# Performance work log

Measured on AMD Instinct MI355X. Metric: run time of the kernel, lower is better.

## Reference

```python
import jax, jax.numpy as jnp
import numpy as np

B, T, D = 2, 1024, 2048
N, K, H = 16, 4, 128          # num_heads, num_kv_heads, head_dim
TC = 1024                     # cached tokens
S = TC + T
MAX_WAVELENGTH = 10000.0
BIG_NEG = -2.3819763e38


def _apply_rope(x, positions):
    """RoPE: positions [B,L] applied to x [B,L,heads,H]."""
    half = x.shape[-1] // 2
    freq_exponents = (2.0 / x.shape[-1]) * jnp.arange(half, dtype=jnp.float32)
    timescale = MAX_WAVELENGTH ** freq_exponents                      # [H/2]
    radians = (positions.astype(jnp.float32)[..., None] / timescale)[..., None, :]  # [B,L,1,H/2]
    sin, cos = jnp.sin(radians), jnp.cos(radians)
    x1, x2 = jnp.split(x, 2, axis=-1)
    res = jnp.concatenate([x1 * cos - x2 * sin, x2 * cos + x1 * sin], axis=-1)
    return res.astype(x.dtype)


def setup_inputs() -> dict:
    key = jax.random.key(0)
    ks = jax.random.split(key, 8)
    x = jax.random.normal(ks[0], (B, T, D), dtype=jnp.float32)
    # new tokens sit right after the cache
    positions = jnp.broadcast_to(TC + jnp.arange(T, dtype=jnp.int32), (B, T))
    # causal mask over [cache + new]: query t may attend to keys s <= TC + t
    s_idx = jnp.arange(S)[None, :]
    t_idx = jnp.arange(T)[:, None]
    attn_mask = jnp.broadcast_to((s_idx <= TC + t_idx)[None, None, :, :], (B, 1, T, S))
    cache_k = jax.random.normal(ks[1], (B, TC, K, H), dtype=jnp.float32)
    cache_v = jax.random.normal(ks[2], (B, TC, K, H), dtype=jnp.float32)
    # lecun-normal-ish fan-in scaling (fan_in = D for projections, N*H for output)
    w_q = jax.random.normal(ks[3], (N, D, H), dtype=jnp.float32) * (D ** -0.5)
    w_kv = jax.random.normal(ks[4], (2, K, D, H), dtype=jnp.float32) * (D ** -0.5)
    w_out = jax.random.normal(ks[5], (N, H, D), dtype=jnp.float32) * ((N * H) ** -0.5)
    return {"x": x, "positions": positions, "attn_mask": attn_mask,
            "cache_k": cache_k, "cache_v": cache_v,
            "w_q": w_q, "w_kv": w_kv, "w_out": w_out}


def reference(x, positions, attn_mask, cache_k, cache_v, w_q, w_kv, w_out):
    dtype = x.dtype
    # projections (GQA path: num_kv_heads != num_heads)
    q = jnp.einsum('BTD,NDH->BTNH', x, w_q.astype(dtype))
    kv = jnp.einsum('BSD,CKDH->CBSKH', x, w_kv.astype(dtype))
    k_new, v_new = kv[0], kv[1]
    # inline RoPE + query scaling
    q = _apply_rope(q, positions) * (H ** -0.5)
    k_new = _apply_rope(k_new, positions)
    # KV-cache concat
    k = jnp.concatenate([cache_k, k_new], axis=1)   # [B,S,K,H]
    v = jnp.concatenate([cache_v, v_new], axis=1)
    # group heads: B T (K G) H -> B T K G H
    G = N // K
    qg = q.reshape(q.shape[0], q.shape[1], K, G, H)
    logits = jnp.einsum('BTKGH,BSKH->BKGTS', qg, k,
                        preferred_element_type=jnp.float32)
    masked = jnp.where(attn_mask[:, :, None, :, :], logits, BIG_NEG)
    probs = jax.nn.softmax(masked, axis=-1).astype(dtype)
    enc = jnp.einsum('BKGTS,BSKH->BTKGH', probs, v)
    enc = enc.reshape(enc.shape[0], enc.shape[1], N, H)  # B T (K G) H
    out = jnp.einsum('BTNH,NHD->BTD', enc, w_out.astype(dtype))
    return out, k, v
```

## Files before the change

### kernel.cpp

```cpp
#include <hip/hip_runtime.h>

#define B_  2
#define T_  1024
#define D_  2048
#define NH  16
#define KH  4
#define HD  128
#define TC_ 1024
#define S_  2048

typedef __bf16 bf16x4v __attribute__((ext_vector_type(4)));
typedef __bf16 bf16x8v __attribute__((ext_vector_type(8)));
typedef float  f32x4v  __attribute__((ext_vector_type(4)));

__device__ __forceinline__ void async_copy16(void* lds, const void* g) {
    __builtin_amdgcn_global_load_lds(
        (__attribute__((address_space(1))) void*)g,
        (__attribute__((address_space(3))) void*)lds, 16, 0, 0);
}

__global__ void cvt_x(const float* __restrict__ x, __bf16* __restrict__ xb) {
    int i = (blockIdx.x * 256 + threadIdx.x) * 4;
    float4 v = *(const float4*)(x + i);
    bf16x4v o; o[0]=(__bf16)v.x; o[1]=(__bf16)v.y; o[2]=(__bf16)v.z; o[3]=(__bf16)v.w;
    *(bf16x4v*)(xb + i) = o;
}

__global__ void tp_w(const float* __restrict__ in, __bf16* __restrict__ out) {
    __shared__ float tile[32][33];
    int h0 = blockIdx.x * 32;
    int d0 = blockIdx.y * 32;
    const float* ip = in + (size_t)blockIdx.z * (D_ * HD);
    __bf16* op = out + (size_t)blockIdx.z * (D_ * HD);
    int tx = threadIdx.x, ty = threadIdx.y;
    for (int i = 0; i < 32; i += 8)
        tile[ty + i][tx] = ip[(size_t)(d0 + ty + i) * HD + h0 + tx];
    __syncthreads();
    for (int i = 0; i < 32; i += 8)
        op[(size_t)(h0 + ty + i) * D_ + d0 + tx] = (__bf16)tile[tx][ty + i];
}

__global__ void tp_wout(const float* __restrict__ in, __bf16* __restrict__ out) {
    __shared__ float tile[32][33];
    int d0 = blockIdx.x * 32;
    int h0 = blockIdx.y * 32;
    int n  = blockIdx.z;
    const float* ip = in + (size_t)n * (HD * D_);
    int tx = threadIdx.x, ty = threadIdx.y;
    for (int i = 0; i < 32; i += 8)
        tile[ty + i][tx] = ip[(size_t)(h0 + ty + i) * D_ + d0 + tx];
    __syncthreads();
    for (int i = 0; i < 32; i += 8)
        out[(size_t)(d0 + ty + i) * (NH * HD) + n * HD + h0 + tx] = (__bf16)tile[tx][ty + i];
}

__global__ void tp_v(const float* __restrict__ vout, __bf16* __restrict__ vtb) {
    __shared__ float tile[32][33];
    int z = blockIdx.z; int b = z / KH, kh = z % KH;
    int h0 = blockIdx.x * 32;
    int s0 = blockIdx.y * 32;
    const float* ip = vout + ((size_t)b * S_ * KH + kh) * HD;
    int tx = threadIdx.x, ty = threadIdx.y;
    for (int i = 0; i < 32; i += 8)
        tile[ty + i][tx] = ip[(size_t)(s0 + ty + i) * (KH * HD) + h0 + tx];
    __syncthreads();
    __bf16* op = vtb + ((size_t)b * KH + kh) * (size_t)HD * S_;
    for (int i = 0; i < 32; i += 8)
        op[(size_t)(h0 + ty + i) * S_ + s0 + tx] = (__bf16)tile[tx][ty + i];
}

__global__ void copy_cache(const float4* __restrict__ ck, const float4* __restrict__ cv,
                           float* __restrict__ kout, float* __restrict__ vout,
                           __bf16* __restrict__ kb) {
    int i = blockIdx.x * 256 + threadIdx.x;
    int b = i >> 17;
    int r = i & 131071;
    float4 kv = ck[i];
    ((float4*)(kout + (size_t)b * S_ * KH * HD))[r] = kv;
    ((float4*)(vout + (size_t)b * S_ * KH * HD))[r] = cv[i];
    int h4 = r & 31;
    int kh = (r >> 5) & 3;
    int s  = r >> 7;
    bf16x4v o; o[0]=(__bf16)kv.x; o[1]=(__bf16)kv.y; o[2]=(__bf16)kv.z; o[3]=(__bf16)kv.w;
    *(bf16x4v*)(kb + (((size_t)(b * KH + kh) * S_ + s) * HD) + h4 * 4) = o;
}

__global__ __launch_bounds__(256, 2)
void gemm_bt(const __bf16* __restrict__ A, const __bf16* __restrict__ BT,
             float* __restrict__ C, int ldc) {
    __shared__ __bf16 As[128 * 64];
    __shared__ __bf16 Bs[128 * 64];
    const int m0 = blockIdx.x * 128, n0 = blockIdx.y * 128;
    const int tid = threadIdx.x;
    const int wave = tid >> 6, lane = tid & 63;
    const int quad = lane >> 4, l16 = lane & 15;
    const int wm = (wave & 1) * 64, wn = (wave >> 1) * 64;
    const int lrow = lane >> 3;
    const int lsw  = (lane & 7) ^ (lrow & 7);

    f32x4v acc[4][4];
    for (int i = 0; i < 4; i++)
        for (int j = 0; j < 4; j++)
            acc[i][j] = (f32x4v){0.f, 0.f, 0.f, 0.f};

    const __bf16* Abase = A + (size_t)m0 * D_;
    const __bf16* Bbase = BT + (size_t)n0 * D_;

    for (int k0 = 0; k0 < D_; k0 += 64) {
        for (int j = 0; j < 4; j++) {
            int r = wave * 32 + j * 8;
            async_copy16(As + (size_t)r * 64,
                         Abase + (size_t)(r + lrow) * D_ + k0 + lsw * 8);
            async_copy16(Bs + (size_t)r * 64,
                         Bbase + (size_t)(r + lrow) * D_ + k0 + lsw * 8);
        }
        __syncthreads();
        for (int ks = 0; ks < 2; ks++) {
            const int ch = ((ks * 4 + quad) ^ (l16 & 7)) * 8;
            bf16x8v a[4], b[4];
            for (int i = 0; i < 4; i++)
                a[i] = *(const bf16x8v*)(As + (wm + i * 16 + l16) * 64 + ch);
            for (int j = 0; j < 4; j++)
                b[j] = *(const bf16x8v*)(Bs + (wn + j * 16 + l16) * 64 + ch);
            for (int i = 0; i < 4; i++)
                for (int j = 0; j < 4; j++)
                    acc[i][j] = __builtin_amdgcn_mfma_f32_16x16x32_bf16(a[i], b[j], acc[i][j], 0, 0, 0);
        }
        __syncthreads();
    }
    for (int i = 0; i < 4; i++)
        for (int j = 0; j < 4; j++)
            for (int r = 0; r < 4; r++) {
                int row = m0 + wm + i * 16 + quad * 4 + r;
                int col = n0 + wn + j * 16 + l16;
                C[(size_t)row * ldc + col] = acc[i][j][r];
            }
}

__global__ void finish_rope(const float* __restrict__ proj, const int* __restrict__ pos,
                            __bf16* __restrict__ qws, float* __restrict__ kout,
                            float* __restrict__ vout, __bf16* __restrict__ kb) {
    const int tau = blockIdx.x;
    const int b = tau >> 10, t = tau & 1023;
    const float p = (float)pos[tau];
    const float* pr = proj + (size_t)tau * 3072;
    const float qscale = 0.08838834764831845f;
    for (int idx = threadIdx.x; idx < (NH + KH) * 64; idx += 256) {
        int head = idx >> 6;
        int hh = idx & 63;
        float ang = p * __expf(-(float)hh * (9.210340371976184f / 64.0f));
        float sn, cs;
        __sincosf(ang, &sn, &cs);
        if (head < NH) {
            float x1 = pr[head * HD + hh], x2 = pr[head * HD + hh + 64];
            size_t qo = ((size_t)tau * NH + head) * HD;
            qws[qo + hh]      = (__bf16)((x1 * cs - x2 * sn) * qscale);
            qws[qo + hh + 64] = (__bf16)((x2 * cs + x1 * sn) * qscale);
        } else {
            int kh = head - NH;
            float x1 = pr[2048 + kh * HD + hh], x2 = pr[2048 + kh * HD + hh + 64];
            float k1 = x1 * cs - x2 * sn, k2 = x2 * cs + x1 * sn;
            size_t ko = ((size_t)(b * S_ + TC_ + t) * KH + kh) * HD;
            kout[ko + hh]      = k1;
            kout[ko + hh + 64] = k2;
            size_t kbo = ((size_t)(b * KH + kh) * S_ + TC_ + t) * HD;
            kb[kbo + hh]      = (__bf16)k1;
            kb[kbo + hh + 64] = (__bf16)k2;
        }
    }
    for (int idx = threadIdx.x; idx < KH * HD; idx += 256) {
        int kh = idx >> 7, h = idx & 127;
        vout[((size_t)(b * S_ + TC_ + t) * KH + kh) * HD + h] = pr[2560 + kh * HD + h];
    }
}

__global__ __launch_bounds__(512, 1)
void attn(const __bf16* __restrict__ qws, const __bf16* __restrict__ kb,
          const __bf16* __restrict__ vtb, __bf16* __restrict__ enc) {
    __shared__ __bf16 Qs[128 * 128];
    __shared__ __bf16 Ks[128 * 128];
    __shared__ __bf16 Vs[128 * 128];
    __shared__ __bf16 Ps[128 * 128];

    const int t0 = blockIdx.x * 128;
    const int n  = blockIdx.y;
    const int b  = blockIdx.z;
    const int kh = n / (NH / KH);
    const int tid = threadIdx.x, wave = tid >> 6, lane = tid & 63;
    const int quad = lane >> 4, l16 = lane & 15;
    const int wm = wave * 16;
    const int arow = lane >> 4;
    const int acol = lane & 15;

    {
        const __bf16* qtile = qws + ((size_t)(b * T_ + t0) * NH + n) * HD;
        for (int jj = 0; jj < 4; jj++) {
            int r0 = wm + jj * 4;
            int row = r0 + arow;
            async_copy16(Qs + (size_t)r0 * 128,
                         qtile + (size_t)row * (NH * HD) + ((acol ^ (row & 15)) * 8));
        }
    }

    float m_run[4], l_run[4];
    f32x4v o_acc[8];
    for (int r = 0; r < 4; r++) { m_run[r] = -INFINITY; l_run[r] = 0.f; }
    for (int j = 0; j < 8; j++) o_acc[j] = (f32x4v){0.f, 0.f, 0.f, 0.f};

    const int nS = (TC_ + t0 + 128) >> 7;
    const __bf16* kbase = kb  + ((size_t)(b * KH + kh)) * S_ * HD;
    const __bf16* vbase = vtb + ((size_t)(b * KH + kh)) * (size_t)HD * S_;

    for (int st = 0; st < nS; st++) {
        const int s0 = st * 128;
        {
            const __bf16* ktile = kbase + (size_t)s0 * HD;
            for (int jj = 0; jj < 4; jj++) {
                int r0 = wm + jj * 4;
                int row = r0 + arow;
                async_copy16(Ks + (size_t)r0 * 128,
                             ktile + (size_t)row * HD + ((acol ^ (row & 15)) * 8));
            }
        }
        {
            const __bf16* vtile = vbase + s0;
            for (int jj = 0; jj < 4; jj++) {
                int r0 = wm + jj * 4;
                int row = r0 + arow;
                async_copy16(Vs + (size_t)r0 * 128,
                             vtile + (size_t)row * S_ + ((acol ^ (row & 15)) * 8));
            }
        }
        __syncthreads();

        f32x4v sc[8];
        for (int j = 0; j < 8; j++) sc[j] = (f32x4v){0.f, 0.f, 0.f, 0.f};
        for (int ks = 0; ks < 4; ks++) {
            int ch = (ks * 4 + quad) ^ l16;
            bf16x8v a = *(const bf16x8v*)(Qs + (wm + l16) * 128 + ch * 8);
            bf16x8v bb[8];
            for (int j = 0; j < 8; j++)
                bb[j] = *(const bf16x8v*)(Ks + (j * 16 + l16) * 128 + ch * 8);
            for (int j = 0; j < 8; j++)
                sc[j] = __builtin_amdgcn_mfma_f32_16x16x32_bf16(a, bb[j], sc[j], 0, 0, 0);
        }

        if (st == nS - 1) {
            for (int j = 0; j < 8; j++)
                for (int r = 0; r < 4; r++) {
                    int row = wm + quad * 4 + r;
                    int col = j * 16 + l16;
                    if (col > row) sc[j][r] = -3.0e38f;
                }
        }

        for (int r = 0; r < 4; r++) {
            float mx = sc[0][r];
            for (int j = 1; j < 8; j++) mx = fmaxf(mx, sc[j][r]);
            for (int off = 8; off >= 1; off >>= 1) mx = fmaxf(mx, __shfl_xor(mx, off, 64));
            mx = fmaxf(mx, m_run[r]);
            float alpha = __expf(m_run[r] - mx);
            m_run[r] = mx;
            float s = 0.f;
            for (int j = 0; j < 8; j++) {
                float pv = __expf(sc[j][r] - mx);
                sc[j][r] = pv;
                s += pv;
            }
            for (int off = 8; off >= 1; off >>= 1) s += __shfl_xor(s, off, 64);
            l_run[r] = l_run[r] * alpha + s;
            for (int j = 0; j < 8; j++) o_acc[j][r] *= alpha;
        }

        for (int j = 0; j < 8; j++)
            for (int r = 0; r < 4; r++) {
                int row = wm + quad * 4 + r;
                int c = (j * 2 + (l16 >> 3)) ^ (row & 15);
                Ps[row * 128 + c * 8 + (l16 & 7)] = (__bf16)sc[j][r];
            }
        __syncthreads();

        for (int ks = 0; ks < 4; ks++) {
            int ch = (ks * 4 + quad) ^ l16;
            bf16x8v a = *(const bf16x8v*)(Ps + (wm + l16) * 128 + ch * 8);
            bf16x8v bb[8];
            for (int j = 0; j < 8; j++)
                bb[j] = *(const bf16x8v*)(Vs + (j * 16 + l16) * 128 + ch * 8);
            for (int j = 0; j < 8; j++)
                o_acc[j] = __builtin_amdgcn_mfma_f32_16x16x32_bf16(a, bb[j], o_acc[j], 0, 0, 0);
        }
        __syncthreads();
    }

    for (int r = 0; r < 4; r++) {
        float inv = 1.0f / l_run[r];
        int row = wm + quad * 4 + r;
        for (int j = 0; j < 8; j++) {
            int col = j * 16 + l16;
            enc[((size_t)(b * T_ + t0 + row) * NH + n) * HD + col] =
                (__bf16)(o_acc[j][r] * inv);
        }
    }
}

extern "C" void kernel_launch(void* const* d_in, const int* in_sizes, int n_in,
                              void* d_out, int out_size, void* d_ws, size_t ws_size,
                              hipStream_t stream) {
    const float* x       = (const float*)d_in[0];
    const int*   pos     = (const int*)d_in[1];
    const float* cache_k = (const float*)d_in[3];
    const float* cache_v = (const float*)d_in[4];
    const float* w_q     = (const float*)d_in[5];
    const float* w_kv    = (const float*)d_in[6];
    const float* w_out   = (const float*)d_in[7];

    float* out  = (float*)d_out;
    float* kout = out  + (size_t)B_ * T_ * D_;
    float* vout = kout + (size_t)B_ * S_ * KH * HD;

    char* ws = (char*)d_ws;
    __bf16* xb   = (__bf16*)ws;  ws += (size_t)B_ * T_ * D_ * 2;
    __bf16* wt   = (__bf16*)ws;  ws += (size_t)3072 * D_ * 2;
    __bf16* wot  = (__bf16*)ws;  ws += (size_t)D_ * NH * HD * 2;
    float*  proj = (float*)ws;   ws += (size_t)B_ * T_ * 3072 * 4;
    __bf16* qws  = (__bf16*)ws;  ws += (size_t)B_ * T_ * NH * HD * 2;
    __bf16* kbuf = (__bf16*)ws;  ws += (size_t)B_ * S_ * KH * HD * 2;
    __bf16* vtb  = (__bf16*)ws;  ws += (size_t)B_ * S_ * KH * HD * 2;
    __bf16* enc  = (__bf16*)ws;

    cvt_x<<<4096, 256, 0, stream>>>(x, xb);
    tp_w<<<dim3(4, 64, 16), dim3(32, 8), 0, stream>>>(w_q, wt);
    tp_w<<<dim3(4, 64, 8),  dim3(32, 8), 0, stream>>>(w_kv, wt + (size_t)16 * HD * D_);
    tp_wout<<<dim3(64, 4, 16), dim3(32, 8), 0, stream>>>(w_out, wot);
    copy_cache<<<1024, 256, 0, stream>>>((const float4*)cache_k, (const float4*)cache_v, kout, vout, kbuf);
    gemm_bt<<<dim3(16, 24), 256, 0, stream>>>(xb, wt, proj, 3072);
    finish_rope<<<2048, 256, 0, stream>>>(proj, pos, qws, kout, vout, kbuf);
    tp_v<<<dim3(4, 64, 8), dim3(32, 8), 0, stream>>>(vout, vtb);
    attn<<<dim3(8, 16, 2), 512, 0, stream>>>(qws, kbuf, vtb, enc);
    gemm_bt<<<dim3(16, 16), 256, 0, stream>>>(enc, wot, out, 2048);
}
```

Measured before the change: 287.0 us.

## Double-buffer K/V tiles with 64-key steps in attention kernel

The attention kernel now processes keys in 64-wide tiles instead of 128, with double-buffered K and V in shared memory. The next tile's async global-to-LDS copies are issued before computing on the current one, so load latency can overlap the MFMA and softmax work. The P-to-LDS barrier now waits only on LDS counters rather than using a full __syncthreads. Smaller tiles double the loop iterations and the rescaling overhead, and masking now spans the last two tiles.

```diff
diff --git a/kernel.cpp b/kernel.cpp
--- a/kernel.cpp
+++ b/kernel.cpp
@@ -178,9 +178,9 @@
 void attn(const __bf16* __restrict__ qws, const __bf16* __restrict__ kb,
           const __bf16* __restrict__ vtb, __bf16* __restrict__ enc) {
     __shared__ __bf16 Qs[128 * 128];
-    __shared__ __bf16 Ks[128 * 128];
-    __shared__ __bf16 Vs[128 * 128];
-    __shared__ __bf16 Ps[128 * 128];
+    __shared__ __bf16 Ks[2][64 * 128];
+    __shared__ __bf16 Vs[2][128 * 64];
+    __shared__ __bf16 Ps[128 * 64];
 
     const int t0 = blockIdx.x * 128;
     const int n  = blockIdx.y;
@@ -189,80 +189,90 @@
     const int tid = threadIdx.x, wave = tid >> 6, lane = tid & 63;
     const int quad = lane >> 4, l16 = lane & 15;
     const int wm = wave * 16;
-    const int arow = lane >> 4;
-    const int acol = lane & 15;
+
+    const __bf16* kbase = kb  + ((size_t)(b * KH + kh)) * S_ * HD;
+    const __bf16* vbase = vtb + ((size_t)(b * KH + kh)) * (size_t)HD * S_;
 
     {
         const __bf16* qtile = qws + ((size_t)(b * T_ + t0) * NH + n) * HD;
         for (int jj = 0; jj < 4; jj++) {
             int r0 = wm + jj * 4;
-            int row = r0 + arow;
+            int row = r0 + (lane >> 4);
             async_copy16(Qs + (size_t)r0 * 128,
-                         qtile + (size_t)row * (NH * HD) + ((acol ^ (row & 15)) * 8));
-        }
-    }
+                         qtile + (size_t)row * (NH * HD) + (((lane & 15) ^ (row & 15)) * 8));
+        }
+    }
+
+    auto stageK = [&](int buf, int s0) {
+        const __bf16* ktile = kbase + (size_t)s0 * HD;
+        for (int jj = 0; jj < 2; jj++) {
+            int r0 = wave * 8 + jj * 4;
+            int row = r0 + (lane >> 4);
+            async_copy16(&Ks[buf][(size_t)r0 * 128],
+                         ktile + (size_t)row * HD + (((lane & 15) ^ (row & 15)) * 8));
+        }
+    };
+    auto stageV = [&](int buf, int s0) {
+        const __bf16* vtile = vbase + s0;
+        for (int jj = 0; jj < 2; jj++) {
+            int r0 = wave * 16 + jj * 8;
+            int row = r0 + (lane >> 3);
+            async_copy16(&Vs[buf][(size_t)r0 * 64],
+                         vtile + (size_t)row * S_ + (((lane & 7) ^ (row & 7)) * 8));
+        }
+    };
 
     float m_run[4], l_run[4];
     f32x4v o_acc[8];
     for (int r = 0; r < 4; r++) { m_run[r] = -INFINITY; l_run[r] = 0.f; }
     for (int j = 0; j < 8; j++) o_acc[j] = (f32x4v){0.f, 0.f, 0.f, 0.f};
 
-    const int nS = (TC_ + t0 + 128) >> 7;
-    const __bf16* kbase = kb  + ((size_t)(b * KH + kh)) * S_ * HD;
-    const __bf16* vbase = vtb + ((size_t)(b * KH + kh)) * (size_t)HD * S_;
-
+    const int nS = (TC_ + t0 + 128) >> 6;
+
+    stageK(0, 0);
+    stageV(0, 0);
+    __syncthreads();
+
+    int cur = 0;
     for (int st = 0; st < nS; st++) {
-        const int s0 = st * 128;
-        {
-            const __bf16* ktile = kbase + (size_t)s0 * HD;
-            for (int jj = 0; jj < 4; jj++) {
-                int r0 = wm + jj * 4;
-                int row = r0 + arow;
-                async_copy16(Ks + (size_t)r0 * 128,
-                             ktile + (size_t)row * HD + ((acol ^ (row & 15)) * 8));
-            }
-        }
-        {
-            const __bf16* vtile = vbase + s0;
-            for (int jj = 0; jj < 4; jj++) {
-                int r0 = wm + jj * 4;
-                int row = r0 + arow;
-                async_copy16(Vs + (size_t)r0 * 128,
-                             vtile + (size_t)row * S_ + ((acol ^ (row & 15)) * 8));
-            }
-        }
-        __syncthreads();
-
-        f32x4v sc[8];
-        for (int j = 0; j < 8; j++) sc[j] = (f32x4v){0.f, 0.f, 0.f, 0.f};
+        const int s0 = st * 64;
+
+        if (st + 1 < nS) {
+            stageK(cur ^ 1, s0 + 64);
+            stageV(cur ^ 1, s0 + 64);
+        }
+
+        f32x4v sc[4];
+        for (int j = 0; j < 4; j++) sc[j] = (f32x4v){0.f, 0.f, 0.f, 0.f};
         for (int ks = 0; ks < 4; ks++) {
-            int ch = (ks * 4 + quad) ^ l16;
-            bf16x8v a = *(const bf16x8v*)(Qs + (wm + l16) * 128 + ch * 8);
-            bf16x8v bb[8];
-            for (int j = 0; j < 8; j++)
-                bb[j] = *(const bf16x8v*)(Ks + (j * 16 + l16) * 128 + ch * 8);
-            for (int j = 0; j < 8; j++)
+            int ch = ((ks * 4 + quad) ^ l16) * 8;
+            bf16x8v a = *(const bf16x8v*)(Qs + (wm + l16) * 128 + ch);
+            bf16x8v bb[4];
+            for (int j = 0; j < 4; j++)
+                bb[j] = *(const bf16x8v*)(&Ks[cur][(j * 16 + l16) * 128 + ch]);
+            for (int j = 0; j < 4; j++)
                 sc[j] = __builtin_amdgcn_mfma_f32_16x16x32_bf16(a, bb[j], sc[j], 0, 0, 0);
         }
 
-        if (st == nS - 1) {
-            for (int j = 0; j < 8; j++)
+        if (st >= nS - 2) {
+            int off = s0 - (TC_ + t0);
+            for (int j = 0; j < 4; j++)
                 for (int r = 0; r < 4; r++) {
                     int row = wm + quad * 4 + r;
                     int col = j * 16 + l16;
-                    if (col > row) sc[j][r] = -3.0e38f;
+                    if (off + col > row) sc[j][r] = -3.0e38f;
                 }
         }
 
         for (int r = 0; r < 4; r++) {
             float mx = sc[0][r];
-            for (int j = 1; j < 8; j++) mx = fmaxf(mx, sc[j][r]);
+            for (int j = 1; j < 4; j++) mx = fmaxf(mx, sc[j][r]);
             for (int off = 8; off >= 1; off >>= 1) mx = fmaxf(mx, __shfl_xor(mx, off, 64));
             mx = fmaxf(mx, m_run[r]);
             float alpha = __expf(m_run[r] - mx);
             m_run[r] = mx;
             float s = 0.f;
-            for (int j = 0; j < 8; j++) {
+            for (int j = 0; j < 4; j++) {
                 float pv = __expf(sc[j][r] - mx);
                 sc[j][r] = pv;
                 s += pv;
@@ -272,24 +282,30 @@
             for (int j = 0; j < 8; j++) o_acc[j][r] *= alpha;
         }
 
-        for (int j = 0; j < 8; j++)
+        for (int j = 0; j < 4; j++)
             for (int r = 0; r < 4; r++) {
                 int row = wm + quad * 4 + r;
-                int c = (j * 2 + (l16 >> 3)) ^ (row & 15);
-                Ps[row * 128 + c * 8 + (l16 & 7)] = (__bf16)sc[j][r];
+                int c = (j * 2 + (l16 >> 3)) ^ (row & 7);
+                Ps[row * 64 + c * 8 + (l16 & 7)] = (__bf16)sc[j][r];
             }
-        __syncthreads();
-
-        for (int ks = 0; ks < 4; ks++) {
-            int ch = (ks * 4 + quad) ^ l16;
-            bf16x8v a = *(const bf16x8v*)(Ps + (wm + l16) * 128 + ch * 8);
+
+        asm volatile("s_waitcnt lgkmcnt(0)" ::: "memory");
+        __builtin_amdgcn_s_barrier();
+        asm volatile("" ::: "memory");
+        __builtin_amdgcn_sched_barrier(0);
+
+        for (int ks = 0; ks < 2; ks++) {
+            int ch = ((ks * 4 + quad) ^ (l16 & 7)) * 8;
+            bf16x8v a = *(const bf16x8v*)(Ps + (wm + l16) * 64 + ch);
             bf16x8v bb[8];
             for (int j = 0; j < 8; j++)
-                bb[j] = *(const bf16x8v*)(Vs + (j * 16 + l16) * 128 + ch * 8);
+                bb[j] = *(const bf16x8v*)(&Vs[cur][(j * 16 + l16) * 64 + ch]);
             for (int j = 0; j < 8; j++)
                 o_acc[j] = __builtin_amdgcn_mfma_f32_16x16x32_bf16(a, bb[j], o_acc[j], 0, 0, 0);
         }
+
         __syncthreads();
+        cur ^= 1;
     }
 
     for (int r = 0; r < 4; r++) {
```

Result: slower. 295.2 us (+2.9%).

## Double-buffer K tiles, prefetch V, and keep Q fragments in registers

Applied to the files above, without the earlier changes.

The attention kernel now loads the Q fragments straight from global memory into registers once, which removes the Q LDS tile and its per-tile LDS reads. K tiles are double-buffered: the next K tile is issued asynchronously before the QK^T MFMAs of the current tile. The next V tile is issued right after the PV step. A hand-placed s_waitcnt vmcnt(4) plus a raw barrier replaces one __syncthreads, so the in-flight K prefetch does not stall the PV phase. This hides global-load latency behind compute, at the cost of more LDS for the second K buffer and more register pressure.

```diff
diff --git a/kernel.cpp b/kernel.cpp
--- a/kernel.cpp
+++ b/kernel.cpp
@@ -177,8 +177,7 @@
 __global__ __launch_bounds__(512, 1)
 void attn(const __bf16* __restrict__ qws, const __bf16* __restrict__ kb,
           const __bf16* __restrict__ vtb, __bf16* __restrict__ enc) {
-    __shared__ __bf16 Qs[128 * 128];
-    __shared__ __bf16 Ks[128 * 128];
+    __shared__ __bf16 Ks[2][128 * 128];
     __shared__ __bf16 Vs[128 * 128];
     __shared__ __bf16 Ps[128 * 128];
 
@@ -192,15 +191,35 @@
     const int arow = lane >> 4;
     const int acol = lane & 15;
 
+    const __bf16* kbase = kb  + ((size_t)(b * KH + kh)) * S_ * HD;
+    const __bf16* vbase = vtb + ((size_t)(b * KH + kh)) * (size_t)HD * S_;
+
+    bf16x8v qreg[4];
     {
-        const __bf16* qtile = qws + ((size_t)(b * T_ + t0) * NH + n) * HD;
+        const __bf16* qrow = qws + ((size_t)(b * T_ + t0 + wm + l16) * NH + n) * HD;
+#pragma unroll
+        for (int ks = 0; ks < 4; ks++)
+            qreg[ks] = *(const bf16x8v*)(qrow + (ks * 4 + quad) * 8);
+    }
+
+    auto stageK = [&](int buf, int s0) {
+        const __bf16* ktile = kbase + (size_t)s0 * HD;
         for (int jj = 0; jj < 4; jj++) {
             int r0 = wm + jj * 4;
             int row = r0 + arow;
-            async_copy16(Qs + (size_t)r0 * 128,
-                         qtile + (size_t)row * (NH * HD) + ((acol ^ (row & 15)) * 8));
-        }
-    }
+            async_copy16(&Ks[buf][(size_t)r0 * 128],
+                         ktile + (size_t)row * HD + ((acol ^ (row & 15)) * 8));
+        }
+    };
+    auto stageV = [&](int s0) {
+        const __bf16* vtile = vbase + s0;
+        for (int jj = 0; jj < 4; jj++) {
+            int r0 = wm + jj * 4;
+            int row = r0 + arow;
+            async_copy16(Vs + (size_t)r0 * 128,
+                         vtile + (size_t)row * S_ + ((acol ^ (row & 15)) * 8));
+        }
+    };
 
     float m_run[4], l_run[4];
     f32x4v o_acc[8];
@@ -208,41 +227,25 @@
     for (int j = 0; j < 8; j++) o_acc[j] = (f32x4v){0.f, 0.f, 0.f, 0.f};
 
     const int nS = (TC_ + t0 + 128) >> 7;
-    const __bf16* kbase = kb  + ((size_t)(b * KH + kh)) * S_ * HD;
-    const __bf16* vbase = vtb + ((size_t)(b * KH + kh)) * (size_t)HD * S_;
-
+
+    stageK(0, 0);
+    stageV(0);
+    __syncthreads();
+
+    int buf = 0;
     for (int st = 0; st < nS; st++) {
-        const int s0 = st * 128;
-        {
-            const __bf16* ktile = kbase + (size_t)s0 * HD;
-            for (int jj = 0; jj < 4; jj++) {
-                int r0 = wm + jj * 4;
-                int row = r0 + arow;
-                async_copy16(Ks + (size_t)r0 * 128,
-                             ktile + (size_t)row * HD + ((acol ^ (row & 15)) * 8));
-            }
-        }
-        {
-            const __bf16* vtile = vbase + s0;
-            for (int jj = 0; jj < 4; jj++) {
-                int r0 = wm + jj * 4;
-                int row = r0 + arow;
-                async_copy16(Vs + (size_t)r0 * 128,
-                             vtile + (size_t)row * S_ + ((acol ^ (row & 15)) * 8));
-            }
-        }
-        __syncthreads();
+        if (st + 1 < nS) stageK(buf ^ 1, (st + 1) * 128);
 
         f32x4v sc[8];
         for (int j = 0; j < 8; j++) sc[j] = (f32x4v){0.f, 0.f, 0.f, 0.f};
+#pragma unroll
         for (int ks = 0; ks < 4; ks++) {
             int ch = (ks * 4 + quad) ^ l16;
-            bf16x8v a = *(const bf16x8v*)(Qs + (wm + l16) * 128 + ch * 8);
             bf16x8v bb[8];
             for (int j = 0; j < 8; j++)
-                bb[j] = *(const bf16x8v*)(Ks + (j * 16 + l16) * 128 + ch * 8);
-            for (int j = 0; j < 8; j++)
-                sc[j] = __builtin_amdgcn_mfma_f32_16x16x32_bf16(a, bb[j], sc[j], 0, 0, 0);
+                bb[j] = *(const bf16x8v*)(&Ks[buf][(j * 16 + l16) * 128 + ch * 8]);
+            for (int j = 0; j < 8; j++)
+                sc[j] = __builtin_amdgcn_mfma_f32_16x16x32_bf16(qreg[ks], bb[j], sc[j], 0, 0, 0);
         }
 
         if (st == nS - 1) {
@@ -278,8 +281,12 @@
                 int c = (j * 2 + (l16 >> 3)) ^ (row & 15);
                 Ps[row * 128 + c * 8 + (l16 & 7)] = (__bf16)sc[j][r];
             }
-        __syncthreads();
-
+
+        asm volatile("s_waitcnt vmcnt(4) lgkmcnt(0)" ::: "memory");
+        __builtin_amdgcn_s_barrier();
+        __builtin_amdgcn_sched_barrier(0);
+
+#pragma unroll
         for (int ks = 0; ks < 4; ks++) {
             int ch = (ks * 4 + quad) ^ l16;
             bf16x8v a = *(const bf16x8v*)(Ps + (wm + l16) * 128 + ch * 8);
@@ -289,7 +296,10 @@
             for (int j = 0; j < 8; j++)
                 o_acc[j] = __builtin_amdgcn_mfma_f32_16x16x32_bf16(a, bb[j], o_acc[j], 0, 0, 0);
         }
+
         __syncthreads();
+        if (st + 1 < nS) stageV((st + 1) * 128);
+        buf ^= 1;
     }
 
     for (int r = 0; r < 4; r++) {
```

Measured after the change: 281.5 us. No clear change (-1.9%).

## Split attention KV range across two blocks and merge partials in combine kernel

Applied to the files above, without the earlier changes.

The attention kernel now processes 256 query rows per block, with each wave owning 32 rows and Q held in registers instead of LDS. The key range is split into two halves handled by separate blocks (split-K style), each writing unnormalized fp32 partial outputs plus running max and sum. A new combine kernel merges the two halves into the bf16 encoding. The intent is to reuse each staged K/V tile across more queries and to balance the causal workload, at the cost of extra fp32 partial traffic, an extra launch, and higher register pressure under launch_bounds(512,2).

```diff
diff --git a/kernel.cpp b/kernel.cpp
--- a/kernel.cpp
+++ b/kernel.cpp
@@ -174,133 +174,184 @@
     }
 }
 
-__global__ __launch_bounds__(512, 1)
+__global__ __launch_bounds__(512, 2)
 void attn(const __bf16* __restrict__ qws, const __bf16* __restrict__ kb,
-          const __bf16* __restrict__ vtb, __bf16* __restrict__ enc) {
-    __shared__ __bf16 Qs[128 * 128];
+          const __bf16* __restrict__ vtb, float* __restrict__ o0,
+          float* __restrict__ o1, float* __restrict__ ml) {
     __shared__ __bf16 Ks[128 * 128];
     __shared__ __bf16 Vs[128 * 128];
-    __shared__ __bf16 Ps[128 * 128];
-
-    const int t0 = blockIdx.x * 128;
+    __shared__ __bf16 Ps[256 * 128];
+
+    const int t0 = blockIdx.x * 256;
     const int n  = blockIdx.y;
-    const int b  = blockIdx.z;
+    const int z  = blockIdx.z;
+    const int b  = z >> 1, sp = z & 1;
     const int kh = n / (NH / KH);
     const int tid = threadIdx.x, wave = tid >> 6, lane = tid & 63;
     const int quad = lane >> 4, l16 = lane & 15;
-    const int wm = wave * 16;
+    const int wm = wave * 32;
+    const int sw = wave * 16;
     const int arow = lane >> 4;
     const int acol = lane & 15;
 
-    {
-        const __bf16* qtile = qws + ((size_t)(b * T_ + t0) * NH + n) * HD;
-        for (int jj = 0; jj < 4; jj++) {
-            int r0 = wm + jj * 4;
-            int row = r0 + arow;
-            async_copy16(Qs + (size_t)r0 * 128,
-                         qtile + (size_t)row * (NH * HD) + ((acol ^ (row & 15)) * 8));
-        }
-    }
-
-    float m_run[4], l_run[4];
-    f32x4v o_acc[8];
-    for (int r = 0; r < 4; r++) { m_run[r] = -INFINITY; l_run[r] = 0.f; }
-    for (int j = 0; j < 8; j++) o_acc[j] = (f32x4v){0.f, 0.f, 0.f, 0.f};
-
-    const int nS = (TC_ + t0 + 128) >> 7;
     const __bf16* kbase = kb  + ((size_t)(b * KH + kh)) * S_ * HD;
     const __bf16* vbase = vtb + ((size_t)(b * KH + kh)) * (size_t)HD * S_;
 
-    for (int st = 0; st < nS; st++) {
+    bf16x8v qreg[2][4];
+#pragma unroll
+    for (int f = 0; f < 2; f++) {
+        const __bf16* qrow = qws + ((size_t)(b * T_ + t0 + wm + f * 16 + l16) * NH + n) * HD;
+#pragma unroll
+        for (int ks = 0; ks < 4; ks++)
+            qreg[f][ks] = *(const bf16x8v*)(qrow + (ks * 4 + quad) * 8);
+    }
+
+    auto stageK = [&](int s0) {
+        const __bf16* ktile = kbase + (size_t)s0 * HD;
+        for (int jj = 0; jj < 4; jj++) {
+            int r0 = sw + jj * 4;
+            int row = r0 + arow;
+            async_copy16(Ks + (size_t)r0 * 128,
+                         ktile + (size_t)row * HD + ((acol ^ (row & 15)) * 8));
+        }
+    };
+    auto stageV = [&](int s0) {
+        const __bf16* vtile = vbase + s0;
+        for (int jj = 0; jj < 4; jj++) {
+            int r0 = sw + jj * 4;
+            int row = r0 + arow;
+            async_copy16(Vs + (size_t)r0 * 128,
+                         vtile + (size_t)row * S_ + ((acol ^ (row & 15)) * 8));
+        }
+    };
+
+    float m_run[2][4], l_run[2][4];
+    f32x4v o_acc[2][8];
+#pragma unroll
+    for (int f = 0; f < 2; f++)
+        for (int r = 0; r < 4; r++) { m_run[f][r] = -INFINITY; l_run[f][r] = 0.f; }
+#pragma unroll
+    for (int f = 0; f < 2; f++)
+        for (int j = 0; j < 8; j++) o_acc[f][j] = (f32x4v){0.f, 0.f, 0.f, 0.f};
+
+    const int nTot = (TC_ + t0 + 256) >> 7;
+    const int half = nTot >> 1;
+    const int stB = sp ? half : 0;
+    const int stE = sp ? nTot : half;
+
+    for (int st = stB; st < stE; st++) {
         const int s0 = st * 128;
-        {
-            const __bf16* ktile = kbase + (size_t)s0 * HD;
-            for (int jj = 0; jj < 4; jj++) {
-                int r0 = wm + jj * 4;
-                int row = r0 + arow;
-                async_copy16(Ks + (size_t)r0 * 128,
-                             ktile + (size_t)row * HD + ((acol ^ (row & 15)) * 8));
-            }
-        }
-        {
-            const __bf16* vtile = vbase + s0;
-            for (int jj = 0; jj < 4; jj++) {
-                int r0 = wm + jj * 4;
-                int row = r0 + arow;
-                async_copy16(Vs + (size_t)r0 * 128,
-                             vtile + (size_t)row * S_ + ((acol ^ (row & 15)) * 8));
-            }
-        }
-        __syncthreads();
-
-        f32x4v sc[8];
-        for (int j = 0; j < 8; j++) sc[j] = (f32x4v){0.f, 0.f, 0.f, 0.f};
+        stageK(s0);
+        stageV(s0);
+        __syncthreads();
+
+        f32x4v sc[2][8];
+#pragma unroll
+        for (int f = 0; f < 2; f++)
+            for (int j = 0; j < 8; j++) sc[f][j] = (f32x4v){0.f, 0.f, 0.f, 0.f};
+#pragma unroll
         for (int ks = 0; ks < 4; ks++) {
             int ch = (ks * 4 + quad) ^ l16;
-            bf16x8v a = *(const bf16x8v*)(Qs + (wm + l16) * 128 + ch * 8);
             bf16x8v bb[8];
+#pragma unroll
             for (int j = 0; j < 8; j++)
                 bb[j] = *(const bf16x8v*)(Ks + (j * 16 + l16) * 128 + ch * 8);
-            for (int j = 0; j < 8; j++)
-                sc[j] = __builtin_amdgcn_mfma_f32_16x16x32_bf16(a, bb[j], sc[j], 0, 0, 0);
-        }
-
-        if (st == nS - 1) {
+#pragma unroll
+            for (int f = 0; f < 2; f++)
+#pragma unroll
+                for (int j = 0; j < 8; j++)
+                    sc[f][j] = __builtin_amdgcn_mfma_f32_16x16x32_bf16(qreg[f][ks], bb[j], sc[f][j], 0, 0, 0);
+        }
+
+        if (st >= nTot - 2) {
+#pragma unroll
+            for (int f = 0; f < 2; f++)
+                for (int j = 0; j < 8; j++)
+                    for (int r = 0; r < 4; r++) {
+                        int row = t0 + wm + f * 16 + quad * 4 + r;
+                        int col = s0 + j * 16 + l16;
+                        if (col > TC_ + row) sc[f][j][r] = -3.0e38f;
+                    }
+        }
+
+#pragma unroll
+        for (int f = 0; f < 2; f++) {
+            for (int r = 0; r < 4; r++) {
+                float mx = sc[f][0][r];
+                for (int j = 1; j < 8; j++) mx = fmaxf(mx, sc[f][j][r]);
+                for (int off = 8; off >= 1; off >>= 1) mx = fmaxf(mx, __shfl_xor(mx, off, 64));
+                mx = fmaxf(mx, m_run[f][r]);
+                float alpha = __expf(m_run[f][r] - mx);
+                m_run[f][r] = mx;
+                float s = 0.f;
+                for (int j = 0; j < 8; j++) {
+                    float pv = __expf(sc[f][j][r] - mx);
+                    sc[f][j][r] = pv;
+                    s += pv;
+                }
+                for (int off = 8; off >= 1; off >>= 1) s += __shfl_xor(s, off, 64);
+                l_run[f][r] = l_run[f][r] * alpha + s;
+                for (int j = 0; j < 8; j++) o_acc[f][j][r] *= alpha;
+            }
             for (int j = 0; j < 8; j++)
                 for (int r = 0; r < 4; r++) {
-                    int row = wm + quad * 4 + r;
-                    int col = j * 16 + l16;
-                    if (col > row) sc[j][r] = -3.0e38f;
+                    int row = wm + f * 16 + quad * 4 + r;
+                    int c = (j * 2 + (l16 >> 3)) ^ (row & 15);
+                    Ps[row * 128 + c * 8 + (l16 & 7)] = (__bf16)sc[f][j][r];
                 }
         }
-
-        for (int r = 0; r < 4; r++) {
-            float mx = sc[0][r];
-            for (int j = 1; j < 8; j++) mx = fmaxf(mx, sc[j][r]);
-            for (int off = 8; off >= 1; off >>= 1) mx = fmaxf(mx, __shfl_xor(mx, off, 64));
-            mx = fmaxf(mx, m_run[r]);
-            float alpha = __expf(m_run[r] - mx);
-            m_run[r] = mx;
-            float s = 0.f;
-            for (int j = 0; j < 8; j++) {
-                float pv = __expf(sc[j][r] - mx);
-                sc[j][r] = pv;
-                s += pv;
-            }
-            for (int off = 8; off >= 1; off >>= 1) s += __shfl_xor(s, off, 64);
-            l_run[r] = l_run[r] * alpha + s;
-            for (int j = 0; j < 8; j++) o_acc[j][r] *= alpha;
-        }
-
-        for (int j = 0; j < 8; j++)
-            for (int r = 0; r < 4; r++) {
-                int row = wm + quad * 4 + r;
-                int c = (j * 2 + (l16 >> 3)) ^ (row & 15);
-                Ps[row * 128 + c * 8 + (l16 & 7)] = (__bf16)sc[j][r];
-            }
-        __syncthreads();
-
+        __syncthreads();
+
+#pragma unroll
         for (int ks = 0; ks < 4; ks++) {
             int ch = (ks * 4 + quad) ^ l16;
-            bf16x8v a = *(const bf16x8v*)(Ps + (wm + l16) * 128 + ch * 8);
+            bf16x8v a0 = *(const bf16x8v*)(Ps + (wm + l16) * 128 + ch * 8);
+            bf16x8v a1 = *(const bf16x8v*)(Ps + (wm + 16 + l16) * 128 + ch * 8);
             bf16x8v bb[8];
+#pragma unroll
             for (int j = 0; j < 8; j++)
                 bb[j] = *(const bf16x8v*)(Vs + (j * 16 + l16) * 128 + ch * 8);
+#pragma unroll
+            for (int j = 0; j < 8; j++) {
+                o_acc[0][j] = __builtin_amdgcn_mfma_f32_16x16x32_bf16(a0, bb[j], o_acc[0][j], 0, 0, 0);
+                o_acc[1][j] = __builtin_amdgcn_mfma_f32_16x16x32_bf16(a1, bb[j], o_acc[1][j], 0, 0, 0);
+            }
+        }
+        __syncthreads();
+    }
+
+    float* op = sp ? o1 : o0;
+#pragma unroll
+    for (int f = 0; f < 2; f++)
+        for (int r = 0; r < 4; r++) {
+            int t = t0 + wm + f * 16 + quad * 4 + r;
+            size_t rowi = ((size_t)(b * T_ + t) * NH + n);
+            float* orow = op + rowi * HD;
             for (int j = 0; j < 8; j++)
-                o_acc[j] = __builtin_amdgcn_mfma_f32_16x16x32_bf16(a, bb[j], o_acc[j], 0, 0, 0);
-        }
-        __syncthreads();
-    }
-
-    for (int r = 0; r < 4; r++) {
-        float inv = 1.0f / l_run[r];
-        int row = wm + quad * 4 + r;
-        for (int j = 0; j < 8; j++) {
-            int col = j * 16 + l16;
-            enc[((size_t)(b * T_ + t0 + row) * NH + n) * HD + col] =
-                (__bf16)(o_acc[j][r] * inv);
-        }
-    }
+                orow[j * 16 + l16] = o_acc[f][j][r];
+            if (l16 == 0) {
+                size_t mli = ((size_t)sp * (B_ * T_ * NH) + rowi) * 2;
+                ml[mli]     = m_run[f][r];
+                ml[mli + 1] = l_run[f][r];
+            }
+        }
+}
+
+__global__ void combine(const float* __restrict__ o0, const float* __restrict__ o1,
+                        const float* __restrict__ ml, __bf16* __restrict__ enc) {
+    int i = blockIdx.x * 256 + threadIdx.x;
+    int row = i >> 5, q = i & 31;
+    float m0 = ml[(size_t)row * 2], l0 = ml[(size_t)row * 2 + 1];
+    float m1 = ml[((size_t)(B_ * T_ * NH) + row) * 2], l1 = ml[((size_t)(B_ * T_ * NH) + row) * 2 + 1];
+    float m = fmaxf(m0, m1);
+    float a0 = __expf(m0 - m), a1 = __expf(m1 - m);
+    float inv = 1.f / (l0 * a0 + l1 * a1);
+    f32x4v v0 = *(const f32x4v*)(o0 + (size_t)row * HD + q * 4);
+    f32x4v v1 = *(const f32x4v*)(o1 + (size_t)row * HD + q * 4);
+    bf16x4v o;
+    for (int k = 0; k < 4; k++)
+        o[k] = (__bf16)((v0[k] * a0 + v1[k] * a1) * inv);
+    *(bf16x4v*)(enc + (size_t)row * HD + q * 4) = o;
 }
 
 extern "C" void kernel_launch(void* const* d_in, const int* in_sizes, int n_in,
@@ -326,7 +377,10 @@
     __bf16* qws  = (__bf16*)ws;  ws += (size_t)B_ * T_ * NH * HD * 2;
     __bf16* kbuf = (__bf16*)ws;  ws += (size_t)B_ * S_ * KH * HD * 2;
     __bf16* vtb  = (__bf16*)ws;  ws += (size_t)B_ * S_ * KH * HD * 2;
-    __bf16* enc  = (__bf16*)ws;
+    __bf16* enc  = (__bf16*)ws;  ws += (size_t)B_ * T_ * NH * HD * 2;
+    float*  o1p  = (float*)ws;   ws += (size_t)B_ * T_ * NH * HD * 4;
+    float*  mlp  = (float*)ws;   ws += (size_t)2 * B_ * T_ * NH * 2 * 4;
+    float*  o0p  = proj;
 
     cvt_x<<<4096, 256, 0, stream>>>(x, xb);
     tp_w<<<dim3(4, 64, 16), dim3(32, 8), 0, stream>>>(w_q, wt);
@@ -336,6 +390,7 @@
     gemm_bt<<<dim3(16, 24), 256, 0, stream>>>(xb, wt, proj, 3072);
     finish_rope<<<2048, 256, 0, stream>>>(proj, pos, qws, kout, vout, kbuf);
     tp_v<<<dim3(4, 64, 8), dim3(32, 8), 0, stream>>>(vout, vtb);
-    attn<<<dim3(8, 16, 2), 512, 0, stream>>>(qws, kbuf, vtb, enc);
+    attn<<<dim3(4, 16, 4), 512, 0, stream>>>(qws, kbuf, vtb, o0p, o1p, mlp);
+    combine<<<4096, 256, 0, stream>>>(o0p, o1p, mlp, enc);
     gemm_bt<<<dim3(16, 16), 256, 0, stream>>>(enc, wot, out, 2048);
 }
```

Result: slower. 353.9 us (+23.3%).
